# Performance work log

Measured on AMD Instinct MI355X. Metric: run time of the kernel, lower is better.

Reference implementation:

```python
import jax, jax.numpy as jnp
import numpy as np

D_MODEL = 1024
N_HEAD = 16
HEAD_DIM = D_MODEL // N_HEAD
LN_EPS = 1e-12


def setup_inputs() -> dict:
    key = jax.random.key(0)
    ks = jax.random.split(key, 9)
    B, S, D = 2, 2048, D_MODEL
    s = 1.0 / np.sqrt(D)
    return {
        "hidden_states": jax.random.normal(ks[0], (B, S, D), jnp.float32),
        "Wq": jax.random.normal(ks[1], (D, D), jnp.float32) * s,
        "bq": jnp.zeros((D,), jnp.float32),
        "Wk": jax.random.normal(ks[2], (D, D), jnp.float32) * s,
        "bk": jnp.zeros((D,), jnp.float32),
        "Wv": jax.random.normal(ks[3], (D, D), jnp.float32) * s,
        "bv": jnp.zeros((D,), jnp.float32),
        "Wo": jax.random.normal(ks[4], (D, D), jnp.float32) * s,
        "bo": jnp.zeros((D,), jnp.float32),
        "ln_gamma": jnp.ones((D,), jnp.float32),
        "ln_beta": jnp.zeros((D,), jnp.float32),
    }


def reference(hidden_states, Wq, bq, Wk, bk, Wv, bv, Wo, bo, ln_gamma, ln_beta):
    # BertAttention forward (eval mode: dropouts are identity).
    B, S, D = hidden_states.shape
    H, Dh = N_HEAD, HEAD_DIM

    def heads(x):  # [B,S,D] -> [B,H,S,Dh]
        return x.reshape(B, S, H, Dh).transpose(0, 2, 1, 3)

    q = heads(hidden_states @ Wq + bq)
    k = heads(hidden_states @ Wk + bk)
    v = heads(hidden_states @ Wv + bv)

    scores = jnp.einsum("bhsd,bhtd->bhst", q, k) / jnp.sqrt(jnp.float32(Dh))
    probs = jax.nn.softmax(scores, axis=-1)
    ctx = jnp.einsum("bhst,bhtd->bhsd", probs, v)
    ctx = ctx.transpose(0, 2, 1, 3).reshape(B, S, D)

    # BertSelfOutput: dense + residual + LayerNorm(eps=1e-12)
    h = ctx @ Wo + bo + hidden_states
    mu = jnp.mean(h, axis=-1, keepdims=True)
    var = jnp.mean(jnp.square(h - mu), axis=-1, keepdims=True)
    out = (h - mu) / jnp.sqrt(var + LN_EPS) * ln_gamma + ln_beta
    return out
```

## Files before the change

kernel.cpp:

```cpp
#include <hip/hip_runtime.h>
#include <hip/hip_bf16.h>

#define D_MODEL 1024
#define N_HEAD  16
#define HEAD_DIM 64
#define BATCH   2
#define SEQ     2048
#define M_ROWS  (BATCH * SEQ)

typedef unsigned short u16;
typedef unsigned int   u32;

typedef __attribute__((ext_vector_type(8))) short bfrag8;
typedef __attribute__((ext_vector_type(4))) float ffrag4;

__device__ __forceinline__ float bf2f(u16 u) {
    return __uint_as_float(((u32)u) << 16);
}
__device__ __forceinline__ u16 f2bf(float f) {
    u32 x = __float_as_uint(f);
    u32 r = (x + 0x7fffu + ((x >> 16) & 1u)) >> 16;
    return (u16)r;
}
__device__ __forceinline__ u32 pack_bf2_trunc(float lo, float hi) {
    return __builtin_amdgcn_perm(__float_as_uint(hi), __float_as_uint(lo),
                                 0x07060302u);
}
__device__ __forceinline__ float fast_exp2(float x) {
    float r;
    asm("v_exp_f32 %0, %1" : "=v"(r) : "v"(x));
    return r;
}

__device__ __forceinline__ void gl_lds16(const void* g, void* l) {
    __builtin_amdgcn_global_load_lds(
        (const __attribute__((address_space(1))) void*)g,
        (__attribute__((address_space(3))) void*)l, 16, 0, 0);
}

#define Q_PRESCALE 0.18033688011112042f

__device__ __forceinline__ int is_bf16(const u32* gb) {
    return gb[0] != 0x3F800000u;
}

__global__ __launch_bounds__(256) void prep_all(
    const void* w0, const void* w1, const void* w2, const void* w3,
    u16* t0, u16* t1, u16* t2, u16* t3,
    const void* v0, const void* v1, const void* v2, const void* v3,
    const void* v4, const void* v5, u16* __restrict__ vecs,
    const void* xsrc, u16* __restrict__ xdst, int xquads,
    const u32* __restrict__ gb)
{
    const int isbf = is_bf16(gb);
    const int tid = threadIdx.x;
    const int z = blockIdx.z;

    if (z < 4) {
        __shared__ u16 t[32][33];
        const void* srcs[4] = {w0, w1, w2, w3};
        u16* dsts[4] = {t0, t1, t2, t3};
        const void* src = srcs[z];
        u16* dst = dsts[z];
        const int bx = blockIdx.x * 32;
        const int by = blockIdx.y * 32;
        const int tx = tid & 31;
        const int ty = tid >> 5;
#pragma unroll
        for (int r = 0; r < 4; r++) {
            const int row = by + ty * 4 + r;
            u16 v;
            if (isbf) v = ((const u16*)src)[(size_t)row * D_MODEL + bx + tx];
            else      v = f2bf(((const float*)src)[(size_t)row * D_MODEL + bx + tx]);
            t[tx][ty * 4 + r] = v;
        }
        __syncthreads();
#pragma unroll
        for (int r = 0; r < 4; r++) {
            const int n = bx + ty * 4 + r;
            dst[(size_t)n * D_MODEL + by + tx] = t[ty * 4 + r][tx];
        }
        return;
    }

    const int id = blockIdx.y * 32 + blockIdx.x;
    if (id < 6) {
        const void* srcs[6] = {v0, v1, v2, v3, v4, v5};
        const void* src = srcs[id];
        u16* dst = vecs + (size_t)id * D_MODEL;
        if (isbf) {
            ((ushort4*)dst)[tid] = ((const ushort4*)src)[tid];
        } else {
            float4 v = ((const float4*)src)[tid];
            ushort4 o;
            o.x = f2bf(v.x); o.y = f2bf(v.y); o.z = f2bf(v.z); o.w = f2bf(v.w);
            ((ushort4*)dst)[tid] = o;
        }
        return;
    }
    if (isbf) return;
    const int nblk = 32 * 32 - 6;
    for (int i = (id - 6) * 256 + tid; i < xquads; i += nblk * 256) {
        float4 v = ((const float4*)xsrc)[i];
        ushort4 o;
        o.x = f2bf(v.x); o.y = f2bf(v.y); o.z = f2bf(v.z); o.w = f2bf(v.w);
        ((ushort4*)xdst)[i] = o;
    }
}

__global__ __launch_bounds__(256, 2) void qkv_mfma(
    const u16* __restrict__ Xraw, const u16* __restrict__ Xconv,
    const u32* __restrict__ gb,
    const u16* __restrict__ WqT, const u16* __restrict__ bq,
    const u16* __restrict__ WkT, const u16* __restrict__ bk,
    const u16* __restrict__ WvT, const u16* __restrict__ bv,
    u16* __restrict__ Qout, u16* __restrict__ Kout, u16* __restrict__ Vout)
{
    const u16* X = is_bf16(gb) ? Xraw : Xconv;

    __shared__ __align__(16) u16 SMEM[2][20480];

    const int tid  = threadIdx.x;
    const int wave = tid >> 6;
    const int lane = tid & 63;
    const int quad = lane >> 4;
    const int l16  = lane & 15;
    const int l7   = l16 & 7;
    const int m0 = blockIdx.y * 128;
    const int n0 = blockIdx.x * 64;
    const int wr = (wave >> 1) * 64;
    const int wc = (wave & 1) * 32;

    ffrag4 acc[3][4][2];
#pragma unroll
    for (int z = 0; z < 3; z++)
#pragma unroll
        for (int i = 0; i < 4; i++)
#pragma unroll
            for (int j = 0; j < 2; j++) acc[z][i][j] = (ffrag4){0.f, 0.f, 0.f, 0.f};

    const int srow8 = lane >> 3;
    const int scolb = ((lane & 7) ^ srow8) * 16;
    const size_t rstep8 = (size_t)8 * (D_MODEL * 2);
    const char* Ag  = (const char*)X   + (size_t)(m0 + wave * 32 + srow8) * (D_MODEL * 2) + scolb;
    const char* Bg0 = (const char*)WqT + (size_t)(n0 + wave * 16 + srow8) * (D_MODEL * 2) + scolb;
    const char* Bg1 = (const char*)WkT + (size_t)(n0 + wave * 16 + srow8) * (D_MODEL * 2) + scolb;
    const char* Bg2 = (const char*)WvT + (size_t)(n0 + wave * 16 + srow8) * (D_MODEL * 2) + scolb;

#define QKV_STAGE(bufp, kbyte)                                              \
    {                                                                       \
        char* Lb = (char*)SMEM[bufp];                                       \
        _Pragma("unroll")                                                   \
        for (int j = 0; j < 4; j++)                                         \
            gl_lds16(Ag + (kbyte) + j * rstep8,                             \
                     Lb + wave * 4096 + j * 1024);                          \
        _Pragma("unroll")                                                   \
        for (int j = 0; j < 2; j++) {                                       \
            gl_lds16(Bg0 + (kbyte) + j * rstep8,                            \
                     Lb + 16384 + wave * 2048 + j * 1024);                  \
            gl_lds16(Bg1 + (kbyte) + j * rstep8,                            \
                     Lb + 16384 + 8192 + wave * 2048 + j * 1024);           \
            gl_lds16(Bg2 + (kbyte) + j * rstep8,                            \
                     Lb + 16384 + 16384 + wave * 2048 + j * 1024);          \
        }                                                                   \
    }

    QKV_STAGE(0, 0);
    int cur = 0;
    for (int k0 = 0; k0 < D_MODEL; k0 += 64) {
        __syncthreads();
        if (k0 + 64 < D_MODEL) QKV_STAGE(cur ^ 1, (size_t)(k0 + 64) * 2);
        const char* Lb = (const char*)SMEM[cur];
#pragma unroll
        for (int kk = 0; kk < 2; kk++) {
            const int chunk = ((kk * 4 + quad) ^ l7) * 16;
            bfrag8 af[4];
#pragma unroll
            for (int mi = 0; mi < 4; mi++)
                af[mi] = *(const bfrag8*)(Lb + (wr + mi * 16 + l16) * 128 + chunk);
#pragma unroll
            for (int z = 0; z < 3; z++) {
                const char* Bz = Lb + 16384 + z * 8192;
                bfrag8 b0 = *(const bfrag8*)(Bz + (wc + l16) * 128 + chunk);
                bfrag8 b1 = *(const bfrag8*)(Bz + (wc + 16 + l16) * 128 + chunk);
#pragma unroll
                for (int mi = 0; mi < 4; mi++) {
                    acc[z][mi][0] = __builtin_amdgcn_mfma_f32_16x16x32_bf16(af[mi], b0, acc[z][mi][0], 0, 0, 0);
                    acc[z][mi][1] = __builtin_amdgcn_mfma_f32_16x16x32_bf16(af[mi], b1, acc[z][mi][1], 0, 0, 0);
                }
            }
        }
        cur ^= 1;
    }
#undef QKV_STAGE

    __syncthreads();

    const int h = n0 >> 6;
    u16* T = (u16*)SMEM[0] + wave * (16 * 48);
#pragma unroll
    for (int z = 0; z < 2; z++) {
        const u16* bias = (z == 0) ? bq : bk;
        u16* Out        = (z == 0) ? Qout : Kout;
#pragma unroll
        for (int mi = 0; mi < 4; mi++) {
#pragma unroll
            for (int ni = 0; ni < 2; ni++) {
                const int col = ni * 16 + l16;
                const float bia = bf2f(bias[n0 + wc + col]);
#pragma unroll
                for (int r = 0; r < 4; r++) {
                    float v = acc[z][mi][ni][r] + bia;
                    if (z == 0) v *= Q_PRESCALE;
                    T[(quad * 4 + r) * 48 + col] = f2bf(v);
                }
            }
            asm volatile("s_waitcnt lgkmcnt(0)" ::: "memory");
            const int m = m0 + wr + mi * 16 + l16;
            const int b = m >> 11;
            const int s = m & 2047;
            u16* dst = Out + ((size_t)(b * N_HEAD + h) * SEQ + s) * HEAD_DIM
                           + wc + quad * 8;
            *(uint4*)dst = *(const uint4*)&T[l16 * 48 + quad * 8];
        }
    }

#pragma unroll
    for (int mi = 0; mi < 4; mi++) {
        const int mbase = m0 + wr + mi * 16 + quad * 4;
        const int b = mbase >> 11;
        const int s = mbase & 2047;
#pragma unroll
        for (int ni = 0; ni < 2; ni++) {
            const int n = n0 + wc + ni * 16 + l16;
            const float bia = bf2f(bv[n]);
            ushort4 o;
            o.x = f2bf(acc[2][mi][ni][0] + bia);
            o.y = f2bf(acc[2][mi][ni][1] + bia);
            o.z = f2bf(acc[2][mi][ni][2] + bia);
            o.w = f2bf(acc[2][mi][ni][3] + bia);
            *(ushort4*)&Vout[((size_t)(b * N_HEAD * HEAD_DIM + n)) * SEQ + s] = o;
        }
    }
}

__global__ __launch_bounds__(256, 2) void attn_mfma(
    const u16* __restrict__ Q, const u16* __restrict__ K,
    const u16* __restrict__ VT, u16* __restrict__ CTX)
{
    __shared__ __align__(16) u16 Ks[2][4096];
    __shared__ __align__(16) u16 Vs[2][4096];
    __shared__ __align__(16) u16 PQ[8192];

    const int tid  = threadIdx.x;
    const int wave = tid >> 6;
    const int lane = tid & 63;
    const int quad = lane >> 4;
    const int l16  = lane & 15;
    const int l7   = l16 & 7;

    const int b  = blockIdx.z;
    const int h  = blockIdx.y;
    const int q0 = blockIdx.x * 128;

    const size_t headoff = (size_t)(b * N_HEAD + h) * SEQ * HEAD_DIM;
    const u16* Qb  = Q  + headoff;
    const u16* Kb  = K  + headoff;
    const u16* VTb = VT + headoff;

    const int srow = tid >> 2;
    const int sc0  = (tid & 3) * 2;
    const int sd0  = srow * 64 + (((sc0    ) ^ (srow & 7)) << 3);
    const int sd1  = srow * 64 + (((sc0 + 1) ^ (srow & 7)) << 3);

    uint4 ka0 = *(const uint4*)&Kb[(size_t)srow * HEAD_DIM + sc0 * 8];
    uint4 ka1 = *(const uint4*)&Kb[(size_t)srow * HEAD_DIM + sc0 * 8 + 8];
    uint4 va0 = *(const uint4*)&VTb[(size_t)srow * SEQ + sc0 * 8];
    uint4 va1 = *(const uint4*)&VTb[(size_t)srow * SEQ + sc0 * 8 + 8];

    {
        const int qrow = tid >> 1;
        const int qcb  = (tid & 1) * 4;
#pragma unroll
        for (int i = 0; i < 4; i++) {
            uint4 v = *(const uint4*)&Qb[(size_t)(q0 + qrow) * HEAD_DIM + (qcb + i) * 8];
            *(uint4*)&PQ[qrow * 64 + (((qcb + i) ^ (qrow & 7)) << 3)] = v;
        }
    }
    __syncthreads();

    const int wq = wave * 32;
    bfrag8 qa[2][2];
#pragma unroll
    for (int g = 0; g < 2; g++)
#pragma unroll
        for (int ch = 0; ch < 2; ch++)
            qa[g][ch] = *(const bfrag8*)&PQ[(wq + g * 16 + l16) * 64 +
                                            (((ch * 4 + quad) ^ l7) << 3)];
    u16* Pw = &PQ[wave * 2048];

    ffrag4 oacc[2][4];
#pragma unroll
    for (int g = 0; g < 2; g++)
#pragma unroll
        for (int c = 0; c < 4; c++) oacc[g][c] = (ffrag4){0.f, 0.f, 0.f, 0.f};
    float lsum[2] = {0.f, 0.f};

    for (int t0 = 0; t0 < SEQ; t0 += 64) {
        const int buf = (t0 >> 6) & 1;
        u16* Kl = Ks[buf];
        u16* Vl = Vs[buf];
        *(uint4*)&Kl[sd0] = ka0;
        *(uint4*)&Kl[sd1] = ka1;
        *(uint4*)&Vl[sd0] = va0;
        *(uint4*)&Vl[sd1] = va1;
        __syncthreads();

        const int tn = (t0 + 64) & (SEQ - 1);
        ka0 = *(const uint4*)&Kb[(size_t)(tn + srow) * HEAD_DIM + sc0 * 8];
        ka1 = *(const uint4*)&Kb[(size_t)(tn + srow) * HEAD_DIM + sc0 * 8 + 8];
        va0 = *(const uint4*)&VTb[(size_t)srow * SEQ + tn + sc0 * 8];
        va1 = *(const uint4*)&VTb[(size_t)srow * SEQ + tn + sc0 * 8 + 8];

        ffrag4 st[4][2];
        __builtin_amdgcn_s_setprio(1);
#pragma unroll
        for (int c = 0; c < 4; c++) {
            const int kr = (c * 16 + l16) * 64;
            const bfrag8 kb0 = *(const bfrag8*)&Kl[kr + ((quad ^ l7) << 3)];
            const bfrag8 kb1 = *(const bfrag8*)&Kl[kr + (((4 + quad) ^ l7) << 3)];
#pragma unroll
            for (int g = 0; g < 2; g++) {
                ffrag4 a = (ffrag4){0.f, 0.f, 0.f, 0.f};
                a = __builtin_amdgcn_mfma_f32_16x16x32_bf16(kb0, qa[g][0], a, 0, 0, 0);
                a = __builtin_amdgcn_mfma_f32_16x16x32_bf16(kb1, qa[g][1], a, 0, 0, 0);
                st[c][g] = a;
            }
        }
        __builtin_amdgcn_s_setprio(0);

#pragma unroll
        for (int g = 0; g < 2; g++) {
            float part = 0.f;
#pragma unroll
            for (int c = 0; c < 4; c++) {
                const float e0 = fast_exp2(st[c][g][0]);
                const float e1 = fast_exp2(st[c][g][1]);
                const float e2 = fast_exp2(st[c][g][2]);
                const float e3 = fast_exp2(st[c][g][3]);
                part += (e0 + e1) + (e2 + e3);
                uint2 pk;
                pk.x = pack_bf2_trunc(e0, e1);
                pk.y = pack_bf2_trunc(e2, e3);
                const int chunk = 2 * c + (quad >> 1);
                *(uint2*)&Pw[(g * 16 + l16) * 64 + ((chunk ^ l7) << 3) +
                             (quad & 1) * 4] = pk;
            }
            part += __shfl_xor(part, 16);
            part += __shfl_xor(part, 32);
            lsum[g] += part;
        }

        asm volatile("s_waitcnt lgkmcnt(0)" ::: "memory");

        bfrag8 pa[2][2];
#pragma unroll
        for (int g = 0; g < 2; g++)
#pragma unroll
            for (int ch = 0; ch < 2; ch++)
                pa[g][ch] = *(const bfrag8*)&Pw[(g * 16 + l16) * 64 +
                                                (((ch * 4 + quad) ^ l7) << 3)];
        __builtin_amdgcn_s_setprio(1);
#pragma unroll
        for (int c = 0; c < 4; c++) {
            const int vr = (c * 16 + l16) * 64;
            const bfrag8 vb0 = *(const bfrag8*)&Vl[vr + ((quad ^ l7) << 3)];
            const bfrag8 vb1 = *(const bfrag8*)&Vl[vr + (((4 + quad) ^ l7) << 3)];
#pragma unroll
            for (int g = 0; g < 2; g++) {
                oacc[g][c] = __builtin_amdgcn_mfma_f32_16x16x32_bf16(pa[g][0], vb0, oacc[g][c], 0, 0, 0);
                oacc[g][c] = __builtin_amdgcn_mfma_f32_16x16x32_bf16(pa[g][1], vb1, oacc[g][c], 0, 0, 0);
            }
        }
        __builtin_amdgcn_s_setprio(0);
    }

#pragma unroll
    for (int g = 0; g < 2; g++) {
        float linv[4];
#pragma unroll
        for (int r = 0; r < 4; r++)
            linv[r] = 1.0f / __shfl(lsum[g], quad * 4 + r, 16);
#pragma unroll
        for (int c = 0; c < 4; c++) {
#pragma unroll
            for (int r = 0; r < 4; r++) {
                const int row = q0 + wq + g * 16 + quad * 4 + r;
                const int dh  = c * 16 + l16;
                CTX[(size_t)(b * SEQ + row) * D_MODEL + h * HEAD_DIM + dh] =
                    f2bf(oacc[g][c][r] * linv[r]);
            }
        }
    }
}

__global__ __launch_bounds__(256, 2) void out_proj_mfma(
    const u16* __restrict__ CTX, const u16* __restrict__ WoT,
    const u16* __restrict__ bo, const u16* __restrict__ Xraw,
    const u16* __restrict__ Xconv, const u32* __restrict__ gb,
    u16* __restrict__ H)
{
    const u16* X = is_bf16(gb) ? Xraw : Xconv;
    __shared__ __align__(16) u16 SMEM[2][12288];

    const int tid  = threadIdx.x;
    const int wave = tid >> 6;
    const int lane = tid & 63;
    const int quad = lane >> 4;
    const int l16  = lane & 15;
    const int l7   = l16 & 7;
    const int m0 = blockIdx.y * 128;
    const int n0 = blockIdx.x * 64;
    const int wr = (wave >> 1) * 64;
    const int wc = (wave & 1) * 32;

    ffrag4 acc[4][2];
#pragma unroll
    for (int i = 0; i < 4; i++)
#pragma unroll
        for (int j = 0; j < 2; j++) acc[i][j] = (ffrag4){0.f, 0.f, 0.f, 0.f};

    const int srow8 = lane >> 3;
    const int scolb = ((lane & 7) ^ srow8) * 16;
    const size_t rstep8 = (size_t)8 * (D_MODEL * 2);
    const char* Ag = (const char*)CTX + (size_t)(m0 + wave * 32 + srow8) * (D_MODEL * 2) + scolb;
    const char* Wg = (const char*)WoT + (size_t)(n0 + wave * 16 + srow8) * (D_MODEL * 2) + scolb;

#define OP_STAGE(bufp, kbyte)                                               \
    {                                                                       \
        char* Lb = (char*)SMEM[bufp];                                       \
        _Pragma("unroll")                                                   \
        for (int j = 0; j < 4; j++)                                         \
            gl_lds16(Ag + (kbyte) + j * rstep8,                             \
                     Lb + wave * 4096 + j * 1024);                          \
        _Pragma("unroll")                                                   \
        for (int j = 0; j < 2; j++)                                         \
            gl_lds16(Wg + (kbyte) + j * rstep8,                             \
                     Lb + 16384 + wave * 2048 + j * 1024);                  \
    }

    OP_STAGE(0, 0);
    int cur = 0;
    for (int k0 = 0; k0 < D_MODEL; k0 += 64) {
        __syncthreads();
        if (k0 + 64 < D_MODEL) OP_STAGE(cur ^ 1, (size_t)(k0 + 64) * 2);
        const char* Lb = (const char*)SMEM[cur];
#pragma unroll
        for (int kk = 0; kk < 2; kk++) {
            const int chunk = ((kk * 4 + quad) ^ l7) * 16;
            bfrag8 af[4];
#pragma unroll
            for (int mi = 0; mi < 4; mi++)
                af[mi] = *(const bfrag8*)(Lb + (wr + mi * 16 + l16) * 128 + chunk);
            bfrag8 b0 = *(const bfrag8*)(Lb + 16384 + (wc + l16) * 128 + chunk);
            bfrag8 b1 = *(const bfrag8*)(Lb + 16384 + (wc + 16 + l16) * 128 + chunk);
#pragma unroll
            for (int mi = 0; mi < 4; mi++) {
                acc[mi][0] = __builtin_amdgcn_mfma_f32_16x16x32_bf16(af[mi], b0, acc[mi][0], 0, 0, 0);
                acc[mi][1] = __builtin_amdgcn_mfma_f32_16x16x32_bf16(af[mi], b1, acc[mi][1], 0, 0, 0);
            }
        }
        cur ^= 1;
    }
#undef OP_STAGE

    __syncthreads();

    float* T = (float*)SMEM[0] + wave * (16 * 36);
#pragma unroll
    for (int mi = 0; mi < 4; mi++) {
#pragma unroll
        for (int ni = 0; ni < 2; ni++) {
            const int col = ni * 16 + l16;
#pragma unroll
            for (int r = 0; r < 4; r++)
                T[(quad * 4 + r) * 36 + col] = acc[mi][ni][r];
        }
        asm volatile("s_waitcnt lgkmcnt(0)" ::: "memory");
        const int m = m0 + wr + mi * 16 + l16;
        const int c = quad * 8;
        float4 v0 = *(const float4*)&T[l16 * 36 + c];
        float4 v1 = *(const float4*)&T[l16 * 36 + c + 4];
        const int n = n0 + wc + c;
        ushort4 b0 = *(const ushort4*)&bo[n];
        ushort4 b1 = *(const ushort4*)&bo[n + 4];
        ushort4 x0 = *(const ushort4*)&X[(size_t)m * D_MODEL + n];
        ushort4 x1 = *(const ushort4*)&X[(size_t)m * D_MODEL + n + 4];
        u16 o0 = f2bf(v0.x + bf2f(b0.x) + bf2f(x0.x));
        u16 o1 = f2bf(v0.y + bf2f(b0.y) + bf2f(x0.y));
        u16 o2 = f2bf(v0.z + bf2f(b0.z) + bf2f(x0.z));
        u16 o3 = f2bf(v0.w + bf2f(b0.w) + bf2f(x0.w));
        u16 o4 = f2bf(v1.x + bf2f(b1.x) + bf2f(x1.x));
        u16 o5 = f2bf(v1.y + bf2f(b1.y) + bf2f(x1.y));
        u16 o6 = f2bf(v1.z + bf2f(b1.z) + bf2f(x1.z));
        u16 o7 = f2bf(v1.w + bf2f(b1.w) + bf2f(x1.w));
        uint4 ov;
        ov.x = (u32)o0 | ((u32)o1 << 16);
        ov.y = (u32)o2 | ((u32)o3 << 16);
        ov.z = (u32)o4 | ((u32)o5 << 16);
        ov.w = (u32)o6 | ((u32)o7 << 16);
        *(uint4*)&H[(size_t)m * D_MODEL + n] = ov;
    }
}

__global__ __launch_bounds__(256) void ln_kernel(
    const u16* __restrict__ H, const u16* __restrict__ gamma,
    const u16* __restrict__ beta, void* __restrict__ out,
    const u32* __restrict__ gb)
{
    const int isbf = is_bf16(gb);
    const int row = blockIdx.x;
    const int tid = threadIdx.x;
    const u16* hr = H + (size_t)row * D_MODEL;

    ushort4 hv = *(const ushort4*)&hr[tid * 4];
    float v0 = bf2f(hv.x), v1 = bf2f(hv.y), v2 = bf2f(hv.z), v3 = bf2f(hv.w);
    float s  = (v0 + v1) + (v2 + v3);
    float ss = (v0 * v0 + v1 * v1) + (v2 * v2 + v3 * v3);

#pragma unroll
    for (int off = 1; off < 64; off <<= 1) {
        s  += __shfl_xor(s, off);
        ss += __shfl_xor(ss, off);
    }
    __shared__ float sbuf[4], ssbuf[4];
    const int w = tid >> 6;
    if ((tid & 63) == 0) { sbuf[w] = s; ssbuf[w] = ss; }
    __syncthreads();
    s  = sbuf[0] + sbuf[1] + sbuf[2] + sbuf[3];
    ss = ssbuf[0] + ssbuf[1] + ssbuf[2] + ssbuf[3];

    const float mu  = s * (1.f / D_MODEL);
    const float var = ss * (1.f / D_MODEL) - mu * mu;
    const float inv = rsqrtf(var + 1e-12f);

    const int n = tid * 4;
    ushort4 g4 = *(const ushort4*)&gamma[n];
    ushort4 b4 = *(const ushort4*)&beta[n];
    float o0 = (v0 - mu) * inv * bf2f(g4.x) + bf2f(b4.x);
    float o1 = (v1 - mu) * inv * bf2f(g4.y) + bf2f(b4.y);
    float o2 = (v2 - mu) * inv * bf2f(g4.z) + bf2f(b4.z);
    float o3 = (v3 - mu) * inv * bf2f(g4.w) + bf2f(b4.w);

    if (isbf) {
        ushort4 ov;
        ov.x = f2bf(o0); ov.y = f2bf(o1); ov.z = f2bf(o2); ov.w = f2bf(o3);
        *(ushort4*)&((u16*)out)[(size_t)row * D_MODEL + n] = ov;
    } else {
        *(float4*)&((float*)out)[(size_t)row * D_MODEL + n] =
            make_float4(o0, o1, o2, o3);
    }
}

extern "C" void kernel_launch(void* const* d_in, const int* in_sizes, int n_in,
                              void* d_out, int out_size, void* d_ws, size_t ws_size,
                              hipStream_t stream) {
    const size_t NTOK = (size_t)M_ROWS * D_MODEL;
    const size_t NW   = (size_t)D_MODEL * D_MODEL;
    const size_t NV   = D_MODEL;

    char* wp = (char*)d_ws;
    u16* Xc   = (u16*)wp;                 wp += NTOK * 2;
    u16* WqT  = (u16*)wp;                 wp += NW * 2;
    u16* WkT  = (u16*)wp;                 wp += NW * 2;
    u16* WvT  = (u16*)wp;                 wp += NW * 2;
    u16* WoT  = (u16*)wp;                 wp += NW * 2;
    u16* vecs = (u16*)wp;                 wp += 6 * NV * 2;
    u16* Q    = (u16*)wp;                 wp += NTOK * 2;
    u16* Kt   = (u16*)wp;                 wp += NTOK * 2;
    u16* Vt   = (u16*)wp;                 wp += NTOK * 2;
    u16* H    = Q;
    u16* CTX  = (u16*)d_out;

    u16* bqc = vecs + 0 * NV;
    u16* bkc = vecs + 1 * NV;
    u16* bvc = vecs + 2 * NV;
    u16* boc = vecs + 3 * NV;
    u16* gc  = vecs + 4 * NV;
    u16* bc  = vecs + 5 * NV;

    const u16* Xraw = (const u16*)d_in[0];
    const u32* gb   = (const u32*)d_in[9];

    prep_all<<<dim3(32, 32, 5), 256, 0, stream>>>(
        d_in[1], d_in[3], d_in[5], d_in[7], WqT, WkT, WvT, WoT,
        d_in[2], d_in[4], d_in[6], d_in[8], d_in[9], d_in[10], vecs,
        d_in[0], Xc, (int)(NTOK / 4), gb);

    qkv_mfma<<<dim3(D_MODEL / 64, M_ROWS / 128), 256, 0, stream>>>(
        Xraw, Xc, gb, WqT, bqc, WkT, bkc, WvT, bvc, Q, Kt, Vt);
    attn_mfma<<<dim3(SEQ / 128, N_HEAD, BATCH), 256, 0, stream>>>(Q, Kt, Vt, CTX);
    out_proj_mfma<<<dim3(D_MODEL / 64, M_ROWS / 128), 256, 0, stream>>>(
        CTX, WoT, boc, Xraw, Xc, gb, H);
    ln_kernel<<<M_ROWS, 256, 0, stream>>>(H, gc, bc, d_out, gb);
}
```

Baseline: 192.6 us.

## Use 32x32 MFMA in attention with register-resident P via permlane32 swap

The attention kernel moves from 16x16x32 to 32x32x16 bf16 MFMA tiles. Q fragments now load straight from global memory into registers. The softmax probabilities are rearranged between lanes with permlane32_swap instead of being written to and re-read from LDS. This removes the P/Q LDS buffer and its wait, and the row-sum shuffles shrink to a single xor. Separately, the weight transpose in prep_all now uses 64x64 tiles with vectorized 16-byte loads and stores, and the x conversion writes 8-element packets. The trade-off is more register pressure from the 16-wide accumulators and the reliance on a newer cross-lane intrinsic.

```diff
diff --git a/kernel.cpp b/kernel.cpp
--- a/kernel.cpp
+++ b/kernel.cpp
@@ -11,8 +11,11 @@
 typedef unsigned short u16;
 typedef unsigned int   u32;
 
-typedef __attribute__((ext_vector_type(8))) short bfrag8;
-typedef __attribute__((ext_vector_type(4))) float ffrag4;
+typedef __attribute__((ext_vector_type(8)))  short bfrag8;
+typedef __attribute__((ext_vector_type(4)))  float ffrag4;
+typedef __attribute__((ext_vector_type(16))) float ffrag16;
+typedef __attribute__((ext_vector_type(4)))  u32   u32x4;
+typedef __attribute__((ext_vector_type(2)))  u32   u32x2;
 
 __device__ __forceinline__ float bf2f(u16 u) {
     return __uint_as_float(((u32)u) << 16);
@@ -57,33 +60,48 @@
     const int z = blockIdx.z;
 
     if (z < 4) {
-        __shared__ u16 t[32][33];
+        __shared__ __align__(16) u16 T[64 * 72];
         const void* srcs[4] = {w0, w1, w2, w3};
         u16* dsts[4] = {t0, t1, t2, t3};
         const void* src = srcs[z];
         u16* dst = dsts[z];
-        const int bx = blockIdx.x * 32;
-        const int by = blockIdx.y * 32;
-        const int tx = tid & 31;
-        const int ty = tid >> 5;
-#pragma unroll
-        for (int r = 0; r < 4; r++) {
-            const int row = by + ty * 4 + r;
-            u16 v;
-            if (isbf) v = ((const u16*)src)[(size_t)row * D_MODEL + bx + tx];
-            else      v = f2bf(((const float*)src)[(size_t)row * D_MODEL + bx + tx]);
-            t[tx][ty * 4 + r] = v;
-        }
+        const int bx = blockIdx.x * 64;
+        const int by = blockIdx.y * 64;
+        const int r  = tid >> 2;
+        const int cb = (tid & 3) * 16;
+
+        u16 v16[16];
+        if (isbf) {
+            const u16* s16 = (const u16*)src + (size_t)(by + r) * D_MODEL + bx + cb;
+            *(uint4*)&v16[0] = *(const uint4*)&s16[0];
+            *(uint4*)&v16[8] = *(const uint4*)&s16[8];
+        } else {
+            const float* sf = (const float*)src + (size_t)(by + r) * D_MODEL + bx + cb;
+#pragma unroll
+            for (int i = 0; i < 4; i++) {
+                float4 v = *(const float4*)&sf[i * 4];
+                v16[i * 4 + 0] = f2bf(v.x);
+                v16[i * 4 + 1] = f2bf(v.y);
+                v16[i * 4 + 2] = f2bf(v.z);
+                v16[i * 4 + 3] = f2bf(v.w);
+            }
+        }
+#pragma unroll
+        for (int i = 0; i < 16; i++)
+            T[(cb + i) * 72 + r] = v16[i];
         __syncthreads();
-#pragma unroll
-        for (int r = 0; r < 4; r++) {
-            const int n = bx + ty * 4 + r;
-            dst[(size_t)n * D_MODEL + by + tx] = t[ty * 4 + r][tx];
-        }
+
+        const int n  = tid >> 2;
+        const int kb = (tid & 3) * 16;
+        uint4 o0 = *(const uint4*)&T[n * 72 + kb];
+        uint4 o1 = *(const uint4*)&T[n * 72 + kb + 8];
+        u16* dr = dst + (size_t)(bx + n) * D_MODEL + by + kb;
+        *(uint4*)&dr[0] = o0;
+        *(uint4*)&dr[8] = o1;
         return;
     }
 
-    const int id = blockIdx.y * 32 + blockIdx.x;
+    const int id = blockIdx.y * 16 + blockIdx.x;
     if (id < 6) {
         const void* srcs[6] = {v0, v1, v2, v3, v4, v5};
         const void* src = srcs[id];
@@ -99,12 +117,17 @@
         return;
     }
     if (isbf) return;
-    const int nblk = 32 * 32 - 6;
-    for (int i = (id - 6) * 256 + tid; i < xquads; i += nblk * 256) {
-        float4 v = ((const float4*)xsrc)[i];
-        ushort4 o;
-        o.x = f2bf(v.x); o.y = f2bf(v.y); o.z = f2bf(v.z); o.w = f2bf(v.w);
-        ((ushort4*)xdst)[i] = o;
+    const int nblk = 16 * 16 - 6;
+    const int xocts = xquads >> 1;
+    for (int i = (id - 6) * 256 + tid; i < xocts; i += nblk * 256) {
+        float4 a = ((const float4*)xsrc)[2 * i];
+        float4 c = ((const float4*)xsrc)[2 * i + 1];
+        uint4 o;
+        o.x = (u32)f2bf(a.x) | ((u32)f2bf(a.y) << 16);
+        o.y = (u32)f2bf(a.z) | ((u32)f2bf(a.w) << 16);
+        o.z = (u32)f2bf(c.x) | ((u32)f2bf(c.y) << 16);
+        o.w = (u32)f2bf(c.z) | ((u32)f2bf(c.w) << 16);
+        ((uint4*)xdst)[i] = o;
     }
 }
 
@@ -250,14 +273,13 @@
 {
     __shared__ __align__(16) u16 Ks[2][4096];
     __shared__ __align__(16) u16 Vs[2][4096];
-    __shared__ __align__(16) u16 PQ[8192];
 
     const int tid  = threadIdx.x;
     const int wave = tid >> 6;
     const int lane = tid & 63;
-    const int quad = lane >> 4;
-    const int l16  = lane & 15;
-    const int l7   = l16 & 7;
+    const int l31  = lane & 31;
+    const int hi   = lane >> 5;
+    const int r7   = l31 & 7;
 
     const int b  = blockIdx.z;
     const int h  = blockIdx.y;
@@ -278,33 +300,18 @@
     uint4 va0 = *(const uint4*)&VTb[(size_t)srow * SEQ + sc0 * 8];
     uint4 va1 = *(const uint4*)&VTb[(size_t)srow * SEQ + sc0 * 8 + 8];
 
-    {
-        const int qrow = tid >> 1;
-        const int qcb  = (tid & 1) * 4;
-#pragma unroll
-        for (int i = 0; i < 4; i++) {
-            uint4 v = *(const uint4*)&Qb[(size_t)(q0 + qrow) * HEAD_DIM + (qcb + i) * 8];
-            *(uint4*)&PQ[qrow * 64 + (((qcb + i) ^ (qrow & 7)) << 3)] = v;
-        }
-    }
-    __syncthreads();
-
     const int wq = wave * 32;
-    bfrag8 qa[2][2];
-#pragma unroll
-    for (int g = 0; g < 2; g++)
-#pragma unroll
-        for (int ch = 0; ch < 2; ch++)
-            qa[g][ch] = *(const bfrag8*)&PQ[(wq + g * 16 + l16) * 64 +
-                                            (((ch * 4 + quad) ^ l7) << 3)];
-    u16* Pw = &PQ[wave * 2048];
-
-    ffrag4 oacc[2][4];
-#pragma unroll
-    for (int g = 0; g < 2; g++)
-#pragma unroll
-        for (int c = 0; c < 4; c++) oacc[g][c] = (ffrag4){0.f, 0.f, 0.f, 0.f};
-    float lsum[2] = {0.f, 0.f};
+    const size_t qrow_off = (size_t)(q0 + wq + l31) * HEAD_DIM;
+    bfrag8 qa[4];
+#pragma unroll
+    for (int ks = 0; ks < 4; ks++)
+        qa[ks] = *(const bfrag8*)&Qb[qrow_off + ks * 16 + hi * 8];
+
+    ffrag16 oacc[2];
+#pragma unroll
+    for (int nb = 0; nb < 2; nb++)
+        oacc[nb] = (ffrag16){0,0,0,0,0,0,0,0,0,0,0,0,0,0,0,0};
+    float lsum = 0.f;
 
     for (int t0 = 0; t0 < SEQ; t0 += 64) {
         const int buf = (t0 >> 6) & 1;
@@ -322,86 +329,80 @@
         va0 = *(const uint4*)&VTb[(size_t)srow * SEQ + tn + sc0 * 8];
         va1 = *(const uint4*)&VTb[(size_t)srow * SEQ + tn + sc0 * 8 + 8];
 
-        ffrag4 st[4][2];
+        ffrag16 st[2];
         __builtin_amdgcn_s_setprio(1);
 #pragma unroll
-        for (int c = 0; c < 4; c++) {
-            const int kr = (c * 16 + l16) * 64;
-            const bfrag8 kb0 = *(const bfrag8*)&Kl[kr + ((quad ^ l7) << 3)];
-            const bfrag8 kb1 = *(const bfrag8*)&Kl[kr + (((4 + quad) ^ l7) << 3)];
-#pragma unroll
-            for (int g = 0; g < 2; g++) {
-                ffrag4 a = (ffrag4){0.f, 0.f, 0.f, 0.f};
-                a = __builtin_amdgcn_mfma_f32_16x16x32_bf16(kb0, qa[g][0], a, 0, 0, 0);
-                a = __builtin_amdgcn_mfma_f32_16x16x32_bf16(kb1, qa[g][1], a, 0, 0, 0);
-                st[c][g] = a;
+        for (int kb = 0; kb < 2; kb++) {
+            ffrag16 a = (ffrag16){0,0,0,0,0,0,0,0,0,0,0,0,0,0,0,0};
+#pragma unroll
+            for (int ks = 0; ks < 4; ks++) {
+                const int row = kb * 32 + l31;
+                const bfrag8 kf = *(const bfrag8*)&Kl[row * 64 +
+                                     (((2 * ks + hi) ^ r7) << 3)];
+                a = __builtin_amdgcn_mfma_f32_32x32x16_bf16(kf, qa[ks], a, 0, 0, 0);
             }
+            st[kb] = a;
         }
         __builtin_amdgcn_s_setprio(0);
 
-#pragma unroll
-        for (int g = 0; g < 2; g++) {
-            float part = 0.f;
-#pragma unroll
-            for (int c = 0; c < 4; c++) {
-                const float e0 = fast_exp2(st[c][g][0]);
-                const float e1 = fast_exp2(st[c][g][1]);
-                const float e2 = fast_exp2(st[c][g][2]);
-                const float e3 = fast_exp2(st[c][g][3]);
-                part += (e0 + e1) + (e2 + e3);
-                uint2 pk;
-                pk.x = pack_bf2_trunc(e0, e1);
-                pk.y = pack_bf2_trunc(e2, e3);
-                const int chunk = 2 * c + (quad >> 1);
-                *(uint2*)&Pw[(g * 16 + l16) * 64 + ((chunk ^ l7) << 3) +
-                             (quad & 1) * 4] = pk;
+        u32 W[2][4][2];
+#pragma unroll
+        for (int kb = 0; kb < 2; kb++)
+#pragma unroll
+            for (int m = 0; m < 4; m++)
+#pragma unroll
+                for (int p = 0; p < 2; p++) {
+                    const float e0 = fast_exp2(st[kb][4 * m + 2 * p]);
+                    const float e1 = fast_exp2(st[kb][4 * m + 2 * p + 1]);
+                    lsum += e0 + e1;
+                    W[kb][m][p] = pack_bf2_trunc(e0, e1);
+                }
+        u32x4 paw[4];
+#pragma unroll
+        for (int kb = 0; kb < 2; kb++)
+#pragma unroll
+            for (int s = 0; s < 2; s++)
+#pragma unroll
+                for (int p = 0; p < 2; p++) {
+                    u32x2 sw = __builtin_amdgcn_permlane32_swap(
+                        W[kb][2 * s][p], W[kb][2 * s + 1][p], false, false);
+                    paw[2 * kb + s][p]     = sw.x;
+                    paw[2 * kb + s][2 + p] = sw.y;
+                }
+
+        __builtin_amdgcn_s_setprio(1);
+#pragma unroll
+        for (int nb = 0; nb < 2; nb++) {
+#pragma unroll
+            for (int ks = 0; ks < 4; ks++) {
+                const int row = nb * 32 + l31;
+                const bfrag8 vf = *(const bfrag8*)&Vl[row * 64 +
+                                     (((2 * ks + hi) ^ r7) << 3)];
+                const bfrag8 pa = *(const bfrag8*)&paw[ks];
+                oacc[nb] = __builtin_amdgcn_mfma_f32_32x32x16_bf16(pa, vf, oacc[nb], 0, 0, 0);
             }
-            part += __shfl_xor(part, 16);
-            part += __shfl_xor(part, 32);
-            lsum[g] += part;
-        }
-
-        asm volatile("s_waitcnt lgkmcnt(0)" ::: "memory");
-
-        bfrag8 pa[2][2];
-#pragma unroll
-        for (int g = 0; g < 2; g++)
-#pragma unroll
-            for (int ch = 0; ch < 2; ch++)
-                pa[g][ch] = *(const bfrag8*)&Pw[(g * 16 + l16) * 64 +
-                                                (((ch * 4 + quad) ^ l7) << 3)];
-        __builtin_amdgcn_s_setprio(1);
-#pragma unroll
-        for (int c = 0; c < 4; c++) {
-            const int vr = (c * 16 + l16) * 64;
-            const bfrag8 vb0 = *(const bfrag8*)&Vl[vr + ((quad ^ l7) << 3)];
-            const bfrag8 vb1 = *(const bfrag8*)&Vl[vr + (((4 + quad) ^ l7) << 3)];
-#pragma unroll
-            for (int g = 0; g < 2; g++) {
-                oacc[g][c] = __builtin_amdgcn_mfma_f32_16x16x32_bf16(pa[g][0], vb0, oacc[g][c], 0, 0, 0);
-                oacc[g][c] = __builtin_amdgcn_mfma_f32_16x16x32_bf16(pa[g][1], vb1, oacc[g][c], 0, 0, 0);
-            }
         }
         __builtin_amdgcn_s_setprio(0);
     }
 
-#pragma unroll
-    for (int g = 0; g < 2; g++) {
-        float linv[4];
-#pragma unroll
-        for (int r = 0; r < 4; r++)
-            linv[r] = 1.0f / __shfl(lsum[g], quad * 4 + r, 16);
-#pragma unroll
-        for (int c = 0; c < 4; c++) {
-#pragma unroll
-            for (int r = 0; r < 4; r++) {
-                const int row = q0 + wq + g * 16 + quad * 4 + r;
-                const int dh  = c * 16 + l16;
-                CTX[(size_t)(b * SEQ + row) * D_MODEL + h * HEAD_DIM + dh] =
-                    f2bf(oacc[g][c][r] * linv[r]);
-            }
-        }
-    }
+    lsum += __shfl_xor(lsum, 32);
+    const float linv = 1.0f / lsum;
+    float* fl = (float*)(&Ks[0][0]) + wave * 32;
+    if (lane < 32) fl[l31] = linv;
+    asm volatile("s_waitcnt lgkmcnt(0)" ::: "memory");
+    float li[16];
+#pragma unroll
+    for (int reg = 0; reg < 16; reg++)
+        li[reg] = fl[(reg & 3) + 8 * (reg >> 2) + 4 * hi];
+#pragma unroll
+    for (int nb = 0; nb < 2; nb++)
+#pragma unroll
+        for (int reg = 0; reg < 16; reg++) {
+            const int row = (reg & 3) + 8 * (reg >> 2) + 4 * hi;
+            CTX[(size_t)(b * SEQ + q0 + wq + row) * D_MODEL
+                + h * HEAD_DIM + nb * 32 + l31] =
+                f2bf(oacc[nb][reg] * li[reg]);
+        }
 }
 
 __global__ __launch_bounds__(256, 2) void out_proj_mfma(
@@ -592,7 +593,7 @@
     const u16* Xraw = (const u16*)d_in[0];
     const u32* gb   = (const u32*)d_in[9];
 
-    prep_all<<<dim3(32, 32, 5), 256, 0, stream>>>(
+    prep_all<<<dim3(16, 16, 5), 256, 0, stream>>>(
         d_in[1], d_in[3], d_in[5], d_in[7], WqT, WkT, WvT, WoT,
         d_in[2], d_in[4], d_in[6], d_in[8], d_in[9], d_in[10], vecs,
         d_in[0], Xc, (int)(NTOK / 4), gb);
```

Result: no change. 189.9 us (-1.4%).
